# Kernel optimization log

Measured on AMD Instinct MI355X. Metric: run time of the kernel, lower is better.

## Reference

```python
import jax, jax.numpy as jnp
import numpy as np

# Module config (init_kwargs): kernel_size = (2, 2)
KH, KW = 2, 2


def setup_inputs() -> dict:
    key = jax.random.key(0)
    x = jax.random.normal(key, (32, 64, 64, 64), dtype=jnp.float32)  # NHWC
    return {"input": x}


def reference(input) -> jnp.ndarray:
    # Faithful closed form of the two sparse Conv2DTranspose layers:
    # layer0 kernel w[0,0,o,i]=1 (stride=k)  -> places sum_c(x) on a stride-k grid
    # layer1 kernel w[p,q,o,i]=1 for p<kh,q<kw (stride=1, then crop)
    #   -> broadcasts each grid value over its kxk cell and sums the C equal
    #      input channels, i.e. multiplies by C.
    # Result: out[b,y,x,o] = C * sum_c input[b, y//KH, x//KW, c] for all o.
    B, H, W, C = input.shape
    s = jnp.sum(input, axis=-1, keepdims=True)            # [B,H,W,1]
    up = jnp.repeat(jnp.repeat(s, KH, axis=1), KW, axis=2)  # [B,H*KH,W*KW,1] nearest-neighbour upsample
    out = jnp.broadcast_to(up * C, (B, H * KH, W * KW, C))
    return out
```

## Files before the change

kernel.cpp:

```cpp
#include <hip/hip_runtime.h>
#include <hip/hip_bf16.h>


typedef float f32x4 __attribute__((ext_vector_type(4)));

__global__ __launch_bounds__(256) void Conv2DTransposeNN_kernel(
    const float* __restrict__ in, float* __restrict__ out) {
    const int bid = blockIdx.x;
    const int t   = threadIdx.x;

    __shared__ float s[64];

    const f32x4* in4 = reinterpret_cast<const f32x4*>(in) + (size_t)bid * 1024;

    float partial[4];
#pragma unroll
    for (int j = 0; j < 4; ++j) {
        f32x4 v = __builtin_nontemporal_load(in4 + t + 256 * j);
        partial[j] = (v.x + v.y) + (v.z + v.w);
    }
#pragma unroll
    for (int j = 0; j < 4; ++j) {
#pragma unroll
        for (int m = 1; m < 16; m <<= 1)
            partial[j] += __shfl_xor(partial[j], m);
    }
    if ((t & 15) == 0) {
        const int g = t >> 4;
#pragma unroll
        for (int j = 0; j < 4; ++j)
            s[g + 16 * j] = partial[j] * 64.0f;
    }
    __syncthreads();

    const int b = bid >> 6;
    const int h = bid & 63;
    f32x4* out4 = reinterpret_cast<f32x4*>(out);
    const size_t row0 = (size_t)(b * 128 + 2 * h) * 2048;

#pragma unroll
    for (int k = 0; k < 8; ++k) {
        const int i = t + 256 * k;
        const float v = s[i >> 5];
        f32x4 val = {v, v, v, v};
        __builtin_nontemporal_store(val, out4 + row0 + i);
        __builtin_nontemporal_store(val, out4 + row0 + 2048 + i);
    }
}

extern "C" void kernel_launch(void* const* d_in, const int* in_sizes, int n_in,
                              void* d_out, int out_size, void* d_ws, size_t ws_size,
                              hipStream_t stream) {
    const float* in = (const float*)d_in[0];
    float* out = (float*)d_out;
    Conv2DTransposeNN_kernel<<<2048, 256, 0, stream>>>(in, out);
}
```

Before: 31.75 us.

## Split fused reduce-broadcast into two kernels via workspace, drop nontemporal hints

Splits the single fused kernel into a reduce kernel that writes per-pixel channel sums to a workspace and a broadcast kernel that reads them and writes the upsampled output. A fused fallback is kept for when no workspace is available. Nontemporal loads and stores are also replaced with plain ones. The split is meant to keep the read-heavy and write-heavy phases from interfering, at the cost of a second launch and an extra round trip through global memory.

```diff
diff --git a/kernel.cpp b/kernel.cpp
--- a/kernel.cpp
+++ b/kernel.cpp
@@ -4,19 +4,17 @@
 
 typedef float f32x4 __attribute__((ext_vector_type(4)));
 
-__global__ __launch_bounds__(256) void Conv2DTransposeNN_kernel(
-    const float* __restrict__ in, float* __restrict__ out) {
+__global__ __launch_bounds__(256) void reduce_kernel(
+    const float* __restrict__ in, float* __restrict__ sums) {
     const int bid = blockIdx.x;
     const int t   = threadIdx.x;
-
     __shared__ float s[64];
 
     const f32x4* in4 = reinterpret_cast<const f32x4*>(in) + (size_t)bid * 1024;
-
     float partial[4];
 #pragma unroll
     for (int j = 0; j < 4; ++j) {
-        f32x4 v = __builtin_nontemporal_load(in4 + t + 256 * j);
+        f32x4 v = in4[t + 256 * j];
         partial[j] = (v.x + v.y) + (v.z + v.w);
     }
 #pragma unroll
@@ -32,6 +30,16 @@
             s[g + 16 * j] = partial[j] * 64.0f;
     }
     __syncthreads();
+    if (t < 64) sums[bid * 64 + t] = s[t];
+}
+
+__global__ __launch_bounds__(256) void bcast_kernel(
+    const float* __restrict__ sums, float* __restrict__ out) {
+    const int bid = blockIdx.x;
+    const int t   = threadIdx.x;
+    __shared__ float s[64];
+    if (t < 64) s[t] = sums[bid * 64 + t];
+    __syncthreads();
 
     const int b = bid >> 6;
     const int h = bid & 63;
@@ -43,8 +51,47 @@
         const int i = t + 256 * k;
         const float v = s[i >> 5];
         f32x4 val = {v, v, v, v};
-        __builtin_nontemporal_store(val, out4 + row0 + i);
-        __builtin_nontemporal_store(val, out4 + row0 + 2048 + i);
+        out4[row0 + i]        = val;
+        out4[row0 + 2048 + i] = val;
+    }
+}
+
+__global__ __launch_bounds__(256) void fused_kernel(
+    const float* __restrict__ in, float* __restrict__ out) {
+    const int bid = blockIdx.x;
+    const int t   = threadIdx.x;
+    __shared__ float s[64];
+    const f32x4* in4 = reinterpret_cast<const f32x4*>(in) + (size_t)bid * 1024;
+    float partial[4];
+#pragma unroll
+    for (int j = 0; j < 4; ++j) {
+        f32x4 v = in4[t + 256 * j];
+        partial[j] = (v.x + v.y) + (v.z + v.w);
+    }
+#pragma unroll
+    for (int j = 0; j < 4; ++j) {
+#pragma unroll
+        for (int m = 1; m < 16; m <<= 1)
+            partial[j] += __shfl_xor(partial[j], m);
+    }
+    if ((t & 15) == 0) {
+        const int g = t >> 4;
+#pragma unroll
+        for (int j = 0; j < 4; ++j)
+            s[g + 16 * j] = partial[j] * 64.0f;
+    }
+    __syncthreads();
+    const int b = bid >> 6;
+    const int h = bid & 63;
+    f32x4* out4 = reinterpret_cast<f32x4*>(out);
+    const size_t row0 = (size_t)(b * 128 + 2 * h) * 2048;
+#pragma unroll
+    for (int k = 0; k < 8; ++k) {
+        const int i = t + 256 * k;
+        const float v = s[i >> 5];
+        f32x4 val = {v, v, v, v};
+        out4[row0 + i]        = val;
+        out4[row0 + 2048 + i] = val;
     }
 }
 
@@ -53,5 +100,12 @@
                               hipStream_t stream) {
     const float* in = (const float*)d_in[0];
     float* out = (float*)d_out;
-    Conv2DTransposeNN_kernel<<<2048, 256, 0, stream>>>(in, out);
+    const size_t need = 2048u * 64u * sizeof(float);
+    if (ws_size >= need && d_ws != nullptr) {
+        float* sums = (float*)d_ws;
+        reduce_kernel<<<2048, 256, 0, stream>>>(in, sums);
+        bcast_kernel<<<2048, 256, 0, stream>>>(sums, out);
+    } else {
+        fused_kernel<<<2048, 256, 0, stream>>>(in, out);
+    }
 }
```

After: 31.95 us. About the same (+0.6%).
